# Optimization experiments

Hardware: AMD Instinct MI355X
Metric: run time of the kernel (lower is better)

Reference implementation:

```python
import jax, jax.numpy as jnp
import numpy as np

N_NODES = 50000
NEG_SLOPE = 0.2


def _with_self_loops(edge_index, n):
    loops = jnp.arange(n, dtype=edge_index.dtype)
    src = jnp.concatenate([edge_index[0], loops])
    dst = jnp.concatenate([edge_index[1], loops])
    return src, dst


def _gat_layer(h_in, W, a_src, a_dst, b, src, dst, n):
    # PyG GATConv, heads=1: h = x @ W; alpha_e = softmax_dst(LeakyReLU(a_src.h_src + a_dst.h_dst))
    h = h_in @ W                                   # [N, H]
    es = h @ a_src                                 # [N]
    ed = h @ a_dst                                 # [N]
    logits = jax.nn.leaky_relu(es[src] + ed[dst], NEG_SLOPE)   # [E]
    m = jax.ops.segment_max(logits, dst, num_segments=n)
    m = jnp.where(jnp.isfinite(m), m, 0.0)
    p = jnp.exp(logits - m[dst])
    denom = jax.ops.segment_sum(p, dst, num_segments=n)
    alpha = p / denom[dst]                         # segment softmax over incoming edges
    out = jax.ops.segment_sum(alpha[:, None] * h[src], dst, num_segments=n)
    return out + b


def setup_inputs() -> dict:
    key = jax.random.key(0)
    ks = jax.random.split(key, 20)
    N, E = N_NODES, 600000
    Cin, H, Cout = 128, 128, 64
    inp = {
        'x': jax.random.normal(ks[0], (N, Cin), dtype=jnp.float32),
        'edge_index_x': jax.random.randint(ks[1], (2, E), 0, N, dtype=jnp.int32),
        'edge_index_y': jax.random.randint(ks[2], (2, E), 0, N, dtype=jnp.int32),
        'indices': jax.random.randint(ks[3], (10000,), 0, N, dtype=jnp.int32),
    }
    def gat_params(k, cin, cout):
        k1, k2, k3 = jax.random.split(k, 3)
        s = 1.0 / np.sqrt(cin)
        return (jax.random.normal(k1, (cin, cout), dtype=jnp.float32) * s,
                jax.random.normal(k2, (cout,), dtype=jnp.float32) * s,
                jax.random.normal(k3, (cout,), dtype=jnp.float32) * s,
                jnp.zeros((cout,), dtype=jnp.float32))
    for name, k, cin in [('x1', ks[4], Cin), ('x2', ks[5], H), ('y1', ks[6], Cin), ('y2', ks[7], H)]:
        W, a_s, a_d, b = gat_params(k, cin, H)
        inp['W' + name] = W; inp['as' + name] = a_s; inp['ad' + name] = a_d; inp['b' + name] = b
    s = 1.0 / np.sqrt(2 * H)
    inp['Wfc'] = jax.random.normal(ks[8], (2 * H, H), dtype=jnp.float32) * s
    inp['bfc'] = jnp.zeros((H,), dtype=jnp.float32)
    s = 1.0 / np.sqrt(H)
    inp['Wout'] = jax.random.normal(ks[9], (H, Cout), dtype=jnp.float32) * s
    inp['bout'] = jnp.zeros((Cout,), dtype=jnp.float32)
    return inp


def reference(x, edge_index_x, edge_index_y, indices,
              Wx1, asx1, adx1, bx1, Wx2, asx2, adx2, bx2,
              Wy1, asy1, ady1, by1, Wy2, asy2, ady2, by2,
              Wfc, bfc, Wout, bout):
    n = x.shape[0]
    sx, dx = _with_self_loops(edge_index_x, n)
    sy, dy = _with_self_loops(edge_index_y, n)
    hx = jax.nn.relu(_gat_layer(x, Wx1, asx1, adx1, bx1, sx, dx, n))
    hx = jax.nn.relu(_gat_layer(hx, Wx2, asx2, adx2, bx2, sx, dx, n))
    hy = jax.nn.relu(_gat_layer(x, Wy1, asy1, ady1, by1, sy, dy, n))
    hy = jax.nn.relu(_gat_layer(hy, Wy2, asy2, ady2, by2, sy, dy, n))
    h = jnp.concatenate([hx, hy], axis=1)          # [N, 2H]
    h = jax.nn.relu(h @ Wfc + bfc)
    out = h @ Wout + bout                          # [N, Cout]
    return out[indices]
```

## Files before the change

### kernel.cpp

```cpp
#include <hip/hip_runtime.h>


typedef __attribute__((ext_vector_type(8))) short bf16x8;
typedef __attribute__((ext_vector_type(4))) float f32x4;

#define BKT_CAP 1280
#define CHUNK   8192
#define LDS_CAP 1536

__device__ __forceinline__ unsigned bf16rne(float x) {
  unsigned u = __float_as_uint(x);
  return (u + 0x7fffu + ((u >> 16) & 1u)) >> 16;
}
__device__ __forceinline__ unsigned pack2(float lo, float hi) {
  return bf16rne(lo) | (bf16rne(hi) << 16);
}
__device__ __forceinline__ float bflo(unsigned u) { return __uint_as_float(u << 16); }
__device__ __forceinline__ float bfhi(unsigned u) { return __uint_as_float(u & 0xffff0000u); }

__global__ __launch_bounds__(256) void prep_all_k(
    const float* __restrict__ W0, const float* __restrict__ W1,
    const float* __restrict__ W2, const float* __restrict__ W3,
    const float* __restrict__ W4,
    const float* __restrict__ as0, const float* __restrict__ ad0,
    const float* __restrict__ as1, const float* __restrict__ ad1,
    const float* __restrict__ as2, const float* __restrict__ ad2,
    const float* __restrict__ as3, const float* __restrict__ ad3,
    ushort* __restrict__ wfrALL, float* __restrict__ wsALL,
    int* __restrict__ bktCnt, int nCnt)
{
  int b = blockIdx.x;
  if (b < 384) {
    int e = b * 256 + threadIdx.x;
    const float* W; int le;
    if (e < 65536) { int m = e >> 14; le = e & 16383;
      W = (m == 0) ? W0 : (m == 1) ? W1 : (m == 2) ? W2 : W3; }
    else { le = e - 65536; W = W4; }
    int i = le & 7, lane = (le >> 3) & 63, ct = (le >> 9) & 7, kt = le >> 12;
    int k   = kt * 32 + ((lane >> 4) << 3) + i;
    int col = ct * 16 + (lane & 15);
    wfrALL[e] = (ushort)bf16rne(W[(size_t)k * 128 + col]);
  } else if (b < 386) {
    int layer = (b - 384) * 2 + (threadIdx.x >> 7);
    int k = threadIdx.x & 127;
    const float* W  = (layer == 0) ? W0 : (layer == 1) ? W1 : (layer == 2) ? W2 : W3;
    const float* as_= (layer == 0) ? as0 : (layer == 1) ? as1 : (layer == 2) ? as2 : as3;
    const float* ad_= (layer == 0) ? ad0 : (layer == 1) ? ad1 : (layer == 2) ? ad2 : ad3;
    float s = 0.f, d = 0.f;
    for (int c = 0; c < 128; ++c) {
      float w = W[(size_t)k * 128 + c];
      s += w * as_[c]; d += w * ad_[c];
    }
    wsALL[layer * 256 + k]       = s;
    wsALL[layer * 256 + 128 + k] = d;
  } else {
    int i = (b - 386) * 256 + threadIdx.x;
    if (i < nCnt) bktCnt[i] = 0;
  }
}

__global__ __launch_bounds__(512) void bucket_k(
    const int* __restrict__ srcA, const int* __restrict__ dstA,
    const int* __restrict__ srcB, const int* __restrict__ dstB,
    int* __restrict__ bktCnt, unsigned* __restrict__ bktEdges, int E, int NB)
{
  __shared__ int      hist[800];
  __shared__ int      lbase[801];
  __shared__ int      gbase[800];
  __shared__ int      cur[800];
  __shared__ int      gsum[16], gpre[16];
  __shared__ unsigned staging[CHUNK];

  const int g    = blockIdx.y;
  const int tid  = threadIdx.x;
  const int wv   = tid >> 6;
  const int lane = tid & 63;
  const int start = blockIdx.x * CHUNK;
  const int count = min(CHUNK, E - start);
  const int* src = g ? srcB : srcA;
  const int* dst = g ? dstB : dstA;

  for (int i = tid; i < NB; i += 512) { hist[i] = 0; cur[i] = 0; }
  __syncthreads();

  unsigned pk[CHUNK / 512];
  int      bk[CHUNK / 512];
#pragma unroll
  for (int k = 0; k < CHUNK / 512; ++k) {
    int i = tid + k * 512;
    pk[k] = 0u; bk[k] = -1;
    if (i < count) {
      int s = src[start + i], d = dst[start + i];
      pk[k] = ((unsigned)s << 6) | (unsigned)(d & 63);
      bk[k] = d >> 6;
      atomicAdd(&hist[bk[k]], 1);
    }
  }
  __syncthreads();

  const int ngrp = (NB + 63) >> 6;
  for (int grp = wv; grp < ngrp; grp += 8) {
    int idx = grp * 64 + lane;
    int v = (idx < NB) ? hist[idx] : 0;
    int s = v;
#pragma unroll
    for (int o = 1; o < 64; o <<= 1) {
      int t = __shfl_up(s, o, 64);
      if (lane >= o) s += t;
    }
    if (idx < NB) lbase[idx] = s - v;
    if (lane == 63) gsum[grp] = s;
  }
  __syncthreads();
  if (tid < 64) {
    int v = (tid < ngrp) ? gsum[tid] : 0;
    int s = v;
#pragma unroll
    for (int o = 1; o < 64; o <<= 1) {
      int t = __shfl_up(s, o, 64);
      if (tid >= o) s += t;
    }
    if (tid < ngrp) gpre[tid] = s - v;
  }
  __syncthreads();
  for (int grp = wv; grp < ngrp; grp += 8) {
    int idx = grp * 64 + lane;
    if (idx < NB && grp > 0) lbase[idx] += gpre[grp];
  }
  if (tid == 0) lbase[NB] = count;
  __syncthreads();

  for (int t = tid; t < NB; t += 512) {
    int hcnt = hist[t];
    gbase[t] = hcnt ? atomicAdd(&bktCnt[g * NB + t], hcnt) : 0;
  }
  __syncthreads();

#pragma unroll
  for (int k = 0; k < CHUNK / 512; ++k) {
    if (bk[k] >= 0) {
      int slot = lbase[bk[k]] + atomicAdd(&cur[bk[k]], 1);
      staging[slot] = pk[k];
    }
  }
  __syncthreads();

  for (int s = tid; s < count; s += 512) {
    int lo = 0, hi = NB - 1;
    while (lo < hi) {
      int mid = (lo + hi + 1) >> 1;
      if (lbase[mid] <= s) lo = mid; else hi = mid - 1;
    }
    int ofs = gbase[lo] + (s - lbase[lo]);
    if (ofs < BKT_CAP)
      bktEdges[(size_t)(g * NB + lo) * BKT_CAP + ofs] = staging[s];
  }
}

__global__ __launch_bounds__(256) void mgemm1_k(
    const float* __restrict__ A, const ushort* __restrict__ wfrALL,
    const float* __restrict__ wsALL, ushort* __restrict__ Cb2,
    float* __restrict__ esA, float* __restrict__ edA, int M)
{
  const int g = blockIdx.y;
  const int m = g ? 2 : 0;
  const ushort* wfrag = wfrALL + (size_t)m * 16384;
  const float* ws_s = wsALL + m * 256;
  const float* ws_d = ws_s + 128;
  ushort* Cb = Cb2 + (size_t)g * M * 128;
  float* es = esA + (size_t)g * M;
  float* ed = edA + (size_t)g * M;

  const int tid = threadIdx.x;
  const int w   = tid >> 6;
  const int l   = tid & 63;
  const int rowbase = blockIdx.x * 64 + w * 16;
  const int arow    = rowbase + (l & 15);
  const bool valid  = arow < M;
  const int kofs    = (l >> 4) * 8;
  const float* Ap   = A + (size_t)arow * 128 + kofs;

  f32x4 acc[8];
#pragma unroll
  for (int ct = 0; ct < 8; ++ct) acc[ct] = (f32x4){0.f, 0.f, 0.f, 0.f};
  float esp = 0.f, edp = 0.f;

  for (int kt = 0; kt < 4; ++kt) {
    float4 a0 = make_float4(0.f, 0.f, 0.f, 0.f), a1 = a0;
    if (valid) {
      a0 = *reinterpret_cast<const float4*>(Ap + kt * 32);
      a1 = *reinterpret_cast<const float4*>(Ap + kt * 32 + 4);
    }
    {
      float4 s0 = *reinterpret_cast<const float4*>(ws_s + kt * 32 + kofs);
      float4 s1 = *reinterpret_cast<const float4*>(ws_s + kt * 32 + kofs + 4);
      float4 d0 = *reinterpret_cast<const float4*>(ws_d + kt * 32 + kofs);
      float4 d1 = *reinterpret_cast<const float4*>(ws_d + kt * 32 + kofs + 4);
      esp += a0.x*s0.x + a0.y*s0.y + a0.z*s0.z + a0.w*s0.w
           + a1.x*s1.x + a1.y*s1.y + a1.z*s1.z + a1.w*s1.w;
      edp += a0.x*d0.x + a0.y*d0.y + a0.z*d0.z + a0.w*d0.w
           + a1.x*d1.x + a1.y*d1.y + a1.z*d1.z + a1.w*d1.w;
    }
    bf16x8 af;
    af[0] = (short)bf16rne(a0.x); af[1] = (short)bf16rne(a0.y);
    af[2] = (short)bf16rne(a0.z); af[3] = (short)bf16rne(a0.w);
    af[4] = (short)bf16rne(a1.x); af[5] = (short)bf16rne(a1.y);
    af[6] = (short)bf16rne(a1.z); af[7] = (short)bf16rne(a1.w);
#pragma unroll
    for (int ct = 0; ct < 8; ++ct) {
      bf16x8 bf = *reinterpret_cast<const bf16x8*>(
          wfrag + (((size_t)(kt * 8 + ct) * 64 + l) << 3));
      acc[ct] = __builtin_amdgcn_mfma_f32_16x16x32_bf16(af, bf, acc[ct], 0, 0, 0);
    }
  }

  const int ccol  = l & 15;
  const int crow0 = rowbase + (l >> 4) * 4;
#pragma unroll
  for (int r = 0; r < 4; ++r) {
    int row = crow0 + r;
    if (row < M) {
#pragma unroll
      for (int ct = 0; ct < 8; ++ct)
        Cb[(size_t)row * 128 + ct * 16 + ccol] = (ushort)bf16rne(acc[ct][r]);
    }
  }

  esp += __shfl_xor(esp, 16, 64); esp += __shfl_xor(esp, 32, 64);
  edp += __shfl_xor(edp, 16, 64); edp += __shfl_xor(edp, 32, 64);
  if (l < 16 && valid) { es[arow] = esp; ed[arow] = edp; }
}

__global__ __launch_bounds__(256) void mgemm2_k(
    const ushort* __restrict__ A2, const ushort* __restrict__ wfrALL,
    ushort* __restrict__ Cb2, int M)
{
  const int g = blockIdx.y;
  const int m = g ? 3 : 1;
  const ushort* A = A2 + (size_t)g * M * 128;
  const ushort* wfrag = wfrALL + (size_t)m * 16384;
  ushort* Cb = Cb2 + (size_t)g * M * 128;

  const int tid = threadIdx.x;
  const int w   = tid >> 6;
  const int l   = tid & 63;
  const int rowbase = blockIdx.x * 64 + w * 16;
  const int arow    = rowbase + (l & 15);
  const bool valid  = arow < M;
  const int kofs    = (l >> 4) * 8;
  const ushort* Ap  = A + (size_t)arow * 128 + kofs;

  f32x4 acc[8];
#pragma unroll
  for (int ct = 0; ct < 8; ++ct) acc[ct] = (f32x4){0.f, 0.f, 0.f, 0.f};

  for (int kt = 0; kt < 4; ++kt) {
    bf16x8 af = (bf16x8){0, 0, 0, 0, 0, 0, 0, 0};
    if (valid) af = *reinterpret_cast<const bf16x8*>(Ap + kt * 32);
#pragma unroll
    for (int i = 0; i < 8; ++i) {
      unsigned v = (unsigned short)af[i];
      af[i] = (short)((v & 0x8000u) ? 0u : v);
    }
#pragma unroll
    for (int ct = 0; ct < 8; ++ct) {
      bf16x8 bf = *reinterpret_cast<const bf16x8*>(
          wfrag + (((size_t)(kt * 8 + ct) * 64 + l) << 3));
      acc[ct] = __builtin_amdgcn_mfma_f32_16x16x32_bf16(af, bf, acc[ct], 0, 0, 0);
    }
  }

  const int ccol  = l & 15;
  const int crow0 = rowbase + (l >> 4) * 4;
#pragma unroll
  for (int r = 0; r < 4; ++r) {
    int row = crow0 + r;
    if (row < M) {
#pragma unroll
      for (int ct = 0; ct < 8; ++ct)
        Cb[(size_t)row * 128 + ct * 16 + ccol] = (ushort)bf16rne(acc[ct][r]);
    }
  }
}

__global__ __launch_bounds__(256) void mgemm_fc_k(
    const ushort* __restrict__ hxy, const int* __restrict__ idx,
    const ushort* __restrict__ wfrag, ushort* __restrict__ Cb, int M, int N)
{
  const int tid = threadIdx.x;
  const int w   = tid >> 6;
  const int l   = tid & 63;
  const int rowbase = blockIdx.x * 64 + w * 16;
  const int arow    = rowbase + (l & 15);
  const bool valid  = arow < M;
  const int r       = valid ? idx[arow] : 0;
  const int kofs    = (l >> 4) * 8;

  f32x4 acc[8];
#pragma unroll
  for (int ct = 0; ct < 8; ++ct) acc[ct] = (f32x4){0.f, 0.f, 0.f, 0.f};

  for (int kt = 0; kt < 8; ++kt) {
    const ushort* Ap = (kt < 4)
        ? hxy + (size_t)r * 128 + kt * 32 + kofs
        : hxy + ((size_t)N + r) * 128 + (kt - 4) * 32 + kofs;
    bf16x8 af = (bf16x8){0, 0, 0, 0, 0, 0, 0, 0};
    if (valid) af = *reinterpret_cast<const bf16x8*>(Ap);
#pragma unroll
    for (int i = 0; i < 8; ++i) {
      unsigned v = (unsigned short)af[i];
      af[i] = (short)((v & 0x8000u) ? 0u : v);
    }
#pragma unroll
    for (int ct = 0; ct < 8; ++ct) {
      bf16x8 bf = *reinterpret_cast<const bf16x8*>(
          wfrag + (((size_t)(kt * 8 + ct) * 64 + l) << 3));
      acc[ct] = __builtin_amdgcn_mfma_f32_16x16x32_bf16(af, bf, acc[ct], 0, 0, 0);
    }
  }

  const int ccol  = l & 15;
  const int crow0 = rowbase + (l >> 4) * 4;
#pragma unroll
  for (int rr = 0; rr < 4; ++rr) {
    int row = crow0 + rr;
    if (row < M) {
#pragma unroll
      for (int ct = 0; ct < 8; ++ct)
        Cb[(size_t)row * 128 + ct * 16 + ccol] = (ushort)bf16rne(acc[ct][rr]);
    }
  }
}

__global__ __launch_bounds__(512) void gat_aggr_k(
    const unsigned* __restrict__ bktEdges, const int* __restrict__ bktCnt,
    const float* __restrict__ esIn, const float* __restrict__ edIn,
    const unsigned* __restrict__ h2,
    const float* __restrict__ biasA, const float* __restrict__ biasB,
    unsigned* __restrict__ outb2, const float* __restrict__ wsALL,
    int wsofsA, int wsofsB,
    float* __restrict__ es2, float* __restrict__ ed2, int N, int NB)
{
  __shared__ int   cntL[64];
  __shared__ int   offL[65];
  __shared__ int   curL[64];
  __shared__ int   ssrc[LDS_CAP];
  __shared__ float sp[LDS_CAP];

  const int bid  = blockIdx.x;
  const int xcd  = bid & 7;
  const int g    = xcd >> 2;
  const int B    = (bid >> 3) * 4 + (xcd & 3);
  if (B >= NB) return;
  const int node0 = B * 64;
  const int tid   = threadIdx.x;
  const int wv    = tid >> 6;
  const int lane  = tid & 63;

  const float* es   = esIn + (size_t)g * N;
  const float* ed   = edIn + (size_t)g * N;
  const unsigned* h = h2 + (size_t)g * N * 64;
  const float* bias = g ? biasB : biasA;
  const int wsofs   = g ? wsofsB : wsofsA;

  int cnt = bktCnt[g * NB + B];
  if (cnt > BKT_CAP) cnt = BKT_CAP;
  const unsigned* eb = bktEdges + (size_t)(g * NB + B) * BKT_CAP;

  if (tid < 64) cntL[tid] = 0;
  __syncthreads();
  for (int i = tid; i < cnt; i += 512)
    atomicAdd(&cntL[eb[i] & 63], 1);
  __syncthreads();
  if (wv == 0) {
    int v = cntL[lane];
    int s = v;
#pragma unroll
    for (int o = 1; o < 64; o <<= 1) {
      int t = __shfl_up(s, o, 64);
      if (lane >= o) s += t;
    }
    offL[lane] = s - v;
    if (lane == 63) offL[64] = s;
    curL[lane] = 0;
  }
  __syncthreads();
  for (int i = tid; i < cnt; i += 512) {
    unsigned u = eb[i];
    int sv   = (int)(u >> 6);
    int dloc = (int)(u & 63);
    float l = es[sv] + ed[node0 + dloc];
    l = (l > 0.f) ? l : 0.2f * l;
    int slot = offL[dloc] + atomicAdd(&curL[dloc], 1);
    if (slot < LDS_CAP) { ssrc[slot] = sv; sp[slot] = expf(l); }
  }
  __syncthreads();

  for (int n0 = wv; n0 < 64; n0 += 8) {
    int node = node0 + n0;
    if (node >= N) break;
    int b0 = offL[n0];
    int e1 = offL[n0 + 1]; if (e1 > LDS_CAP) e1 = LDS_CAP;
    float sl_l = es[node] + ed[node];
    sl_l = (sl_l > 0.f) ? sl_l : 0.2f * sl_l;
    float pself = expf(sl_l);
    unsigned u = h[(size_t)node * 64 + lane];
    float ax = pself * bflo(u), ay = pself * bfhi(u);
    float dsum = pself;
    for (int c0 = b0; c0 < e1; c0 += 64) {
      int nc = e1 - c0; if (nc > 64) nc = 64;
      int  sl = ssrc[c0 + (lane < nc ? lane : 0)];
      float pl = (lane < nc) ? sp[c0 + lane] : 0.f;
      float ds = pl;
#pragma unroll
      for (int o = 32; o > 0; o >>= 1) ds += __shfl_xor(ds, o, 64);
      dsum += ds;
      for (int e = 0; e < nc; e += 8) {
        unsigned hv[8]; float pp[8];
#pragma unroll
        for (int k = 0; k < 8; ++k) {
          int s = __builtin_amdgcn_readlane(sl, e + k);
          pp[k] = __int_as_float(__builtin_amdgcn_readlane(__float_as_int(pl), e + k));
          hv[k] = h[(size_t)s * 64 + lane];
        }
#pragma unroll
        for (int k = 0; k < 8; ++k) {
          ax += pp[k] * bflo(hv[k]);
          ay += pp[k] * bfhi(hv[k]);
        }
      }
    }
    float inv = 1.f / dsum;
    float o0 = ax * inv + bias[lane * 2];
    float o1 = ay * inv + bias[lane * 2 + 1];
    outb2[(size_t)g * N * 64 + (size_t)node * 64 + lane] = pack2(o0, o1);
    if (wsofs >= 0) {
      const float* ws_s = wsALL + wsofs;
      const float* ws_d = ws_s + 128;
      float r0 = fmaxf(o0, 0.f), r1 = fmaxf(o1, 0.f);
      float esv = r0 * ws_s[lane * 2] + r1 * ws_s[lane * 2 + 1];
      float edn = r0 * ws_d[lane * 2] + r1 * ws_d[lane * 2 + 1];
#pragma unroll
      for (int o = 32; o > 0; o >>= 1) {
        esv += __shfl_xor(esv, o, 64);
        edn += __shfl_xor(edn, o, 64);
      }
      if (lane == 0) { es2[(size_t)g * N + node] = esv; ed2[(size_t)g * N + node] = edn; }
    }
  }
}

__global__ __launch_bounds__(256) void head_k(
    const unsigned* __restrict__ fcu, const float* __restrict__ bfc,
    const float* __restrict__ Wout, const float* __restrict__ bout,
    float* __restrict__ out, int M)
{
  __shared__ float rowbuf[4][128];
  int widx = threadIdx.x >> 6;
  int lane = threadIdx.x & 63;
  int i = blockIdx.x * 4 + widx;
  if (i >= M) return;
  unsigned u = fcu[(size_t)i * 64 + lane];
  rowbuf[widx][lane * 2]     = fmaxf(bflo(u) + bfc[lane * 2], 0.f);
  rowbuf[widx][lane * 2 + 1] = fmaxf(bfhi(u) + bfc[lane * 2 + 1], 0.f);
  float acc = bout[lane];
#pragma unroll 8
  for (int k = 0; k < 128; ++k) acc += rowbuf[widx][k] * Wout[k * 64 + lane];
  out[(size_t)i * 64 + lane] = acc;
}


extern "C" void kernel_launch(void* const* d_in, const int* in_sizes, int n_in,
                              void* d_out, int out_size, void* d_ws, size_t ws_size,
                              hipStream_t stream)
{
  const float* x    = (const float*)d_in[0];
  const int*   eix  = (const int*)d_in[1];
  const int*   eiy  = (const int*)d_in[2];
  const int*   idx  = (const int*)d_in[3];
  const float* Wx1  = (const float*)d_in[4];
  const float* asx1 = (const float*)d_in[5];
  const float* adx1 = (const float*)d_in[6];
  const float* bx1  = (const float*)d_in[7];
  const float* Wx2  = (const float*)d_in[8];
  const float* asx2 = (const float*)d_in[9];
  const float* adx2 = (const float*)d_in[10];
  const float* bx2  = (const float*)d_in[11];
  const float* Wy1  = (const float*)d_in[12];
  const float* asy1 = (const float*)d_in[13];
  const float* ady1 = (const float*)d_in[14];
  const float* by1  = (const float*)d_in[15];
  const float* Wy2  = (const float*)d_in[16];
  const float* asy2 = (const float*)d_in[17];
  const float* ady2 = (const float*)d_in[18];
  const float* by2  = (const float*)d_in[19];
  const float* Wfc  = (const float*)d_in[20];
  const float* bfc  = (const float*)d_in[21];
  const float* Wout = (const float*)d_in[22];
  const float* bout = (const float*)d_in[23];

  const int N    = in_sizes[0] / 128;
  const int E    = in_sizes[1] / 2;
  const int Midx = in_sizes[3];
  const int NB   = (N + 63) / 64;

  const int* srcx = eix;
  const int* dstx = eix + E;
  const int* srcy = eiy;
  const int* dsty = eiy + E;

  char* p = (char*)d_ws;
  const size_t NH = (size_t)N * 128;
  ushort* hbf2   = (ushort*)p;  p += 2 * NH * 2;
  ushort* inter2 = (ushort*)p;  p += 2 * NH * 2;
  ushort* hxy    = (ushort*)p;  p += 2 * NH * 2;
  float* esA  = (float*)p;      p += (size_t)2 * N * 4;
  float* edA  = (float*)p;      p += (size_t)2 * N * 4;
  float* es2A = (float*)p;      p += (size_t)2 * N * 4;
  float* ed2A = (float*)p;      p += (size_t)2 * N * 4;
  int*   bktCnt = (int*)p;      p += (size_t)2 * NB * 4;
  p = (char*)(((size_t)p + 255) & ~(size_t)255);
  unsigned* bktEdges = (unsigned*)p;  p += (size_t)2 * NB * BKT_CAP * 4;
  ushort* wfrALL = (ushort*)p;  p += 98304 * 2;
  float*  wsALL  = (float*)p;   p += 1024 * 4;

  const int nCnt = 2 * NB;
  const int nz   = (nCnt + 255) / 256;
  const dim3 gBkt((E + CHUNK - 1) / CHUNK, 2);
  const dim3 gGemm((N + 63) / 64, 2);
  const int  gAggr = 8 * ((NB + 3) / 4);

  prep_all_k<<<dim3(386 + nz), 256, 0, stream>>>(Wx1, Wx2, Wy1, Wy2, Wfc,
                                                 asx1, adx1, asx2, adx2,
                                                 asy1, ady1, asy2, ady2,
                                                 wfrALL, wsALL, bktCnt, nCnt);
  bucket_k<<<gBkt, 512, 0, stream>>>(srcx, dstx, srcy, dsty, bktCnt, bktEdges, E, NB);

  mgemm1_k<<<gGemm, 256, 0, stream>>>(x, wfrALL, wsALL, hbf2, esA, edA, N);
  gat_aggr_k<<<dim3(gAggr), 512, 0, stream>>>(bktEdges, bktCnt, esA, edA, (const unsigned*)hbf2,
                                              bx1, by1, (unsigned*)inter2, wsALL,
                                              1 * 256, 3 * 256, es2A, ed2A, N, NB);
  mgemm2_k<<<gGemm, 256, 0, stream>>>(inter2, wfrALL, hbf2, N);
  gat_aggr_k<<<dim3(gAggr), 512, 0, stream>>>(bktEdges, bktCnt, es2A, ed2A, (const unsigned*)hbf2,
                                              bx2, by2, (unsigned*)hxy, wsALL,
                                              -1, -1, nullptr, nullptr, N, NB);

  ushort* fcout = inter2;
  mgemm_fc_k<<<dim3((Midx + 63) / 64), 256, 0, stream>>>(hxy, idx, wfrALL + 65536,
                                                         fcout, Midx, N);
  head_k<<<dim3((Midx + 3) / 4), 256, 0, stream>>>((const unsigned*)fcout, bfc, Wout, bout,
                                                   (float*)d_out, Midx);
}
```

Baseline: 232.1 us.

## Pre-sort bucket edges by destination once and reuse across both GAT layers

Adds a sort_k kernel that counting-sorts each 64-node bucket's edges by local destination once, writing the sorted source ids back in place along with per-bucket offsets. Both gat_aggr_k launches then read these offsets and sorted edges directly instead of each redoing the histogram, scan and scatter in LDS. Edge logits and exp are now computed per lane inside the aggregation loop. This frees most of the LDS, which may allow higher occupancy, and removes duplicated sorting work, at the cost of an extra kernel launch and some global round trips.

```diff
diff --git a/kernel.cpp b/kernel.cpp
--- a/kernel.cpp
+++ b/kernel.cpp
@@ -6,7 +6,6 @@
 
 #define BKT_CAP 1280
 #define CHUNK   8192
-#define LDS_CAP 1536
 
 __device__ __forceinline__ unsigned bf16rne(float x) {
   unsigned u = __float_as_uint(x);
@@ -157,6 +156,53 @@
   }
 }
 
+__global__ __launch_bounds__(512) void sort_k(
+    unsigned* __restrict__ bktEdges, const int* __restrict__ bktCnt,
+    int* __restrict__ offG, int NB)
+{
+  __shared__ int      cntL[64];
+  __shared__ int      offL[65];
+  __shared__ int      curL[64];
+  __shared__ unsigned stage[BKT_CAP];
+
+  const int g   = blockIdx.y;
+  const int B   = blockIdx.x;
+  const int tid = threadIdx.x;
+  int cnt = bktCnt[g * NB + B];
+  if (cnt > BKT_CAP) cnt = BKT_CAP;
+  unsigned* eb = bktEdges + (size_t)(g * NB + B) * BKT_CAP;
+
+  if (tid < 64) cntL[tid] = 0;
+  __syncthreads();
+  for (int i = tid; i < cnt; i += 512)
+    atomicAdd(&cntL[eb[i] & 63], 1);
+  __syncthreads();
+  if (tid < 64) {
+    int v = cntL[tid];
+    int s = v;
+#pragma unroll
+    for (int o = 1; o < 64; o <<= 1) {
+      int t = __shfl_up(s, o, 64);
+      if (tid >= o) s += t;
+    }
+    offL[tid] = s - v;
+    if (tid == 63) offL[64] = s;
+    curL[tid] = 0;
+  }
+  __syncthreads();
+  for (int i = tid; i < cnt; i += 512) {
+    unsigned u = eb[i];
+    int dloc = (int)(u & 63);
+    int slot = offL[dloc] + atomicAdd(&curL[dloc], 1);
+    stage[slot] = u >> 6;
+  }
+  __syncthreads();
+  for (int i = tid; i < cnt; i += 512)
+    eb[i] = stage[i];
+  if (tid < 65)
+    offG[(size_t)(g * NB + B) * 65 + tid] = offL[tid];
+}
+
 __global__ __launch_bounds__(256) void mgemm1_k(
     const float* __restrict__ A, const ushort* __restrict__ wfrALL,
     const float* __restrict__ wsALL, ushort* __restrict__ Cb2,
@@ -333,7 +379,7 @@
 }
 
 __global__ __launch_bounds__(512) void gat_aggr_k(
-    const unsigned* __restrict__ bktEdges, const int* __restrict__ bktCnt,
+    const unsigned* __restrict__ srtEdges, const int* __restrict__ offG,
     const float* __restrict__ esIn, const float* __restrict__ edIn,
     const unsigned* __restrict__ h2,
     const float* __restrict__ biasA, const float* __restrict__ biasB,
@@ -341,11 +387,7 @@
     int wsofsA, int wsofsB,
     float* __restrict__ es2, float* __restrict__ ed2, int N, int NB)
 {
-  __shared__ int   cntL[64];
-  __shared__ int   offL[65];
-  __shared__ int   curL[64];
-  __shared__ int   ssrc[LDS_CAP];
-  __shared__ float sp[LDS_CAP];
+  __shared__ int offL[65];
 
   const int bid  = blockIdx.x;
   const int xcd  = bid & 7;
@@ -362,46 +404,17 @@
   const unsigned* h = h2 + (size_t)g * N * 64;
   const float* bias = g ? biasB : biasA;
   const int wsofs   = g ? wsofsB : wsofsA;
-
-  int cnt = bktCnt[g * NB + B];
-  if (cnt > BKT_CAP) cnt = BKT_CAP;
-  const unsigned* eb = bktEdges + (size_t)(g * NB + B) * BKT_CAP;
-
-  if (tid < 64) cntL[tid] = 0;
-  __syncthreads();
-  for (int i = tid; i < cnt; i += 512)
-    atomicAdd(&cntL[eb[i] & 63], 1);
-  __syncthreads();
-  if (wv == 0) {
-    int v = cntL[lane];
-    int s = v;
-#pragma unroll
-    for (int o = 1; o < 64; o <<= 1) {
-      int t = __shfl_up(s, o, 64);
-      if (lane >= o) s += t;
-    }
-    offL[lane] = s - v;
-    if (lane == 63) offL[64] = s;
-    curL[lane] = 0;
-  }
-  __syncthreads();
-  for (int i = tid; i < cnt; i += 512) {
-    unsigned u = eb[i];
-    int sv   = (int)(u >> 6);
-    int dloc = (int)(u & 63);
-    float l = es[sv] + ed[node0 + dloc];
-    l = (l > 0.f) ? l : 0.2f * l;
-    int slot = offL[dloc] + atomicAdd(&curL[dloc], 1);
-    if (slot < LDS_CAP) { ssrc[slot] = sv; sp[slot] = expf(l); }
-  }
+  const unsigned* eb = srtEdges + (size_t)(g * NB + B) * BKT_CAP;
+
+  if (tid < 65) offL[tid] = offG[(size_t)(g * NB + B) * 65 + tid];
   __syncthreads();
 
   for (int n0 = wv; n0 < 64; n0 += 8) {
     int node = node0 + n0;
     if (node >= N) break;
-    int b0 = offL[n0];
-    int e1 = offL[n0 + 1]; if (e1 > LDS_CAP) e1 = LDS_CAP;
-    float sl_l = es[node] + ed[node];
+    int b0 = offL[n0], e1 = offL[n0 + 1];
+    float edv = ed[node];
+    float sl_l = es[node] + edv;
     sl_l = (sl_l > 0.f) ? sl_l : 0.2f * sl_l;
     float pself = expf(sl_l);
     unsigned u = h[(size_t)node * 64 + lane];
@@ -409,8 +422,13 @@
     float dsum = pself;
     for (int c0 = b0; c0 < e1; c0 += 64) {
       int nc = e1 - c0; if (nc > 64) nc = 64;
-      int  sl = ssrc[c0 + (lane < nc ? lane : 0)];
-      float pl = (lane < nc) ? sp[c0 + lane] : 0.f;
+      int  sl = (int)eb[c0 + (lane < nc ? lane : 0)];
+      float pl = 0.f;
+      if (lane < nc) {
+        float l = es[sl] + edv;
+        l = (l > 0.f) ? l : 0.2f * l;
+        pl = expf(l);
+      }
       float ds = pl;
 #pragma unroll
       for (int o = 32; o > 0; o >>= 1) ds += __shfl_xor(ds, o, 64);
@@ -519,6 +537,7 @@
   float* es2A = (float*)p;      p += (size_t)2 * N * 4;
   float* ed2A = (float*)p;      p += (size_t)2 * N * 4;
   int*   bktCnt = (int*)p;      p += (size_t)2 * NB * 4;
+  int*   offG   = (int*)p;      p += (size_t)2 * NB * 65 * 4;
   p = (char*)(((size_t)p + 255) & ~(size_t)255);
   unsigned* bktEdges = (unsigned*)p;  p += (size_t)2 * NB * BKT_CAP * 4;
   ushort* wfrALL = (ushort*)p;  p += 98304 * 2;
@@ -527,6 +546,7 @@
   const int nCnt = 2 * NB;
   const int nz   = (nCnt + 255) / 256;
   const dim3 gBkt((E + CHUNK - 1) / CHUNK, 2);
+  const dim3 gSrt(NB, 2);
   const dim3 gGemm((N + 63) / 64, 2);
   const int  gAggr = 8 * ((NB + 3) / 4);
 
@@ -535,13 +555,14 @@
                                                  asy1, ady1, asy2, ady2,
                                                  wfrALL, wsALL, bktCnt, nCnt);
   bucket_k<<<gBkt, 512, 0, stream>>>(srcx, dstx, srcy, dsty, bktCnt, bktEdges, E, NB);
+  sort_k<<<gSrt, 512, 0, stream>>>(bktEdges, bktCnt, offG, NB);
 
   mgemm1_k<<<gGemm, 256, 0, stream>>>(x, wfrALL, wsALL, hbf2, esA, edA, N);
-  gat_aggr_k<<<dim3(gAggr), 512, 0, stream>>>(bktEdges, bktCnt, esA, edA, (const unsigned*)hbf2,
+  gat_aggr_k<<<dim3(gAggr), 512, 0, stream>>>(bktEdges, offG, esA, edA, (const unsigned*)hbf2,
                                               bx1, by1, (unsigned*)inter2, wsALL,
                                               1 * 256, 3 * 256, es2A, ed2A, N, NB);
   mgemm2_k<<<gGemm, 256, 0, stream>>>(inter2, wfrALL, hbf2, N);
-  gat_aggr_k<<<dim3(gAggr), 512, 0, stream>>>(bktEdges, bktCnt, es2A, ed2A, (const unsigned*)hbf2,
+  gat_aggr_k<<<dim3(gAggr), 512, 0, stream>>>(bktEdges, offG, es2A, ed2A, (const unsigned*)hbf2,
                                               bx2, by2, (unsigned*)hxy, wsALL,
                                               -1, -1, nullptr, nullptr, N, NB);
 
```

Measured after the change: 238.8 us. 2.9% more time.
